# Optimization experiments

Hardware: AMD Instinct MI355X
Metric: run time of the kernel (lower is better)

The kernel has to match this reference:

```python
import jax, jax.numpy as jnp
import numpy as np

NUM_GRAPHS = 512
NODES_PER_GRAPH = 128
HIDDEN = 64
K = 24


def _param(key, shape, scale=0.05):
    return jax.random.normal(key, shape, dtype=jnp.float32) * scale


def setup_inputs() -> dict:
    key = jax.random.key(0)
    ks = jax.random.split(key, 24)
    N = NUM_GRAPHS * NODES_PER_GRAPH
    inp = {
        "x_pf": jax.random.normal(ks[0], (N, 4), dtype=jnp.float32),
        "batch_pf": jnp.repeat(jnp.arange(NUM_GRAPHS, dtype=jnp.int64), NODES_PER_GRAPH),
        # pf_encode: Linear(4,64), ELU, Linear(64,64), ELU
        "we1": _param(ks[1], (4, HIDDEN)), "be1": _param(ks[2], (HIDDEN,)),
        "we2": _param(ks[3], (HIDDEN, HIDDEN)), "be2": _param(ks[4], (HIDDEN,)),
        # three DynamicEdgeConv edge MLPs: Linear(128,64)+ELU
        "wc1": _param(ks[5], (2 * HIDDEN, HIDDEN)), "bc1": _param(ks[6], (HIDDEN,)),
        "wc2": _param(ks[7], (2 * HIDDEN, HIDDEN)), "bc2": _param(ks[8], (HIDDEN,)),
        "wc3": _param(ks[9], (2 * HIDDEN, HIDDEN)), "bc3": _param(ks[10], (HIDDEN,)),
        # output MLP 64->64->32->32->8->1
        "wo1": _param(ks[11], (HIDDEN, 64)), "bo1": _param(ks[12], (64,)),
        "wo2": _param(ks[13], (64, 32)), "bo2": _param(ks[14], (32,)),
        "wo3": _param(ks[15], (32, 32)), "bo3": _param(ks[16], (32,)),
        "wo4": _param(ks[17], (32, 8)), "bo4": _param(ks[18], (8,)),
        "wo5": _param(ks[19], (8, 1)), "bo5": _param(ks[20], (1,)),
    }
    return inp


def dynamic_edge_conv(x, wc, bc):
    """x: [G,P,D]. kNN (incl. self) in feature space per graph, edge feature
    [x_i, x_j - x_i] -> Linear+ELU -> max over neighbors. Matches PyG
    DynamicEdgeConv(nn, k, aggr='max')."""
    sq = jnp.sum(x * x, axis=-1)                                   # [G,P]
    d = sq[:, :, None] + sq[:, None, :] - 2.0 * jnp.einsum('gpd,gqd->gpq', x, x)
    _, idx = jax.lax.top_k(-d, K)                                   # [G,P,K] nearest (self included, dist 0)
    xj = jax.vmap(lambda xg, ig: xg[ig])(x, idx)                    # [G,P,K,D]
    xi = x[:, :, None, :]
    e = jnp.concatenate([jnp.broadcast_to(xi, xj.shape), xj - xi], axis=-1)  # [G,P,K,2D]
    h = jax.nn.elu(e @ wc + bc)                                     # [G,P,K,D]
    return jnp.max(h, axis=2)                                       # [G,P,D]


def reference(x_pf, batch_pf, we1, be1, we2, be2, wc1, bc1, wc2, bc2, wc3, bc3,
              wo1, bo1, wo2, bo2, wo3, bo3, wo4, bo4, wo5, bo5):
    elu = jax.nn.elu
    h = elu(elu(x_pf @ we1 + be1) @ we2 + be2)                      # [N,64]
    h = h.reshape(NUM_GRAPHS, NODES_PER_GRAPH, HIDDEN)              # equal-size graphs
    h = dynamic_edge_conv(h, wc1, bc1)
    h = dynamic_edge_conv(h, wc2, bc2)
    h = dynamic_edge_conv(h, wc3, bc3)
    pooled = jnp.sum(h, axis=1)                                     # global_add_pool -> [G,64]
    o = elu(pooled @ wo1 + bo1)
    o = elu(o @ wo2 + bo2)
    o = elu(o @ wo3 + bo3)
    o = elu(o @ wo4 + bo4)
    out = o @ wo5 + bo5                                             # [G,1]
    return (out, batch_pf)
```

## Files before the change

### kernel.cpp

```cpp
#include <hip/hip_runtime.h>
#include <math.h>

#define NG 512
#define NP 128
#define HID 64
#define KNN 24
#define NTOT (NG*NP)

typedef __attribute__((ext_vector_type(8)))  short  short8;
typedef __attribute__((ext_vector_type(16))) float  floatx16;

__device__ __forceinline__ float elu_f(float v) { return v > 0.0f ? v : expm1f(v); }

__device__ __forceinline__ void split_bf16(float x, unsigned short& hb, unsigned short& lb) {
    unsigned u = __float_as_uint(x);
    unsigned h = (u + 0x7FFFu + ((u >> 16) & 1u)) >> 16;
    hb = (unsigned short)h;
    float hf = __uint_as_float(h << 16);
    float lo = x - hf;
    unsigned v = __float_as_uint(lo);
    lb = (unsigned short)((v + 0x7FFFu + ((v >> 16) & 1u)) >> 16);
}

__device__ __forceinline__ unsigned short* hchunk(unsigned short* base, int row, int ch) {
    return base + (((row << 4) + (ch ^ (row & 15))) << 3);
}
__device__ __forceinline__ const unsigned short* hchunk(const unsigned short* base, int row, int ch) {
    return base + (((row << 4) + (ch ^ (row & 15))) << 3);
}

__device__ __forceinline__ void sort8_asc(unsigned* y) {
    #pragma unroll
    for (int k = 2; k <= 8; k <<= 1)
        #pragma unroll
        for (int j = k >> 1; j > 0; j >>= 1)
            #pragma unroll
            for (int i = 0; i < 8; ++i) {
                const int l = i ^ j;
                if (l > i) {
                    const bool up = ((i & k) == 0);
                    const unsigned a = y[i], b = y[l];
                    const unsigned mn = a < b ? a : b;
                    const unsigned mx = a < b ? b : a;
                    y[i] = up ? mn : mx;
                    y[l] = up ? mx : mn;
                }
            }
}

__device__ __forceinline__ void merge_top24(unsigned* x) {
    #pragma unroll
    for (int d = 16; d > 0; d >>= 1)
        #pragma unroll
        for (int i = 0; i < 32; ++i)
            if (!(i & d) && i < 24) {
                const int l = i | d;
                const unsigned a = x[i], b = x[l];
                x[i] = a < b ? a : b;
                x[l] = a < b ? b : a;
            }
}

__global__ __launch_bounds__(256) void pack_w(
    const float* __restrict__ wc1, const float* __restrict__ wc2, const float* __restrict__ wc3,
    const float* __restrict__ we2,
    unsigned short* __restrict__ wp)
{
    const int n = blockIdx.x*256 + threadIdx.x;
    if (n < 24576) {
        const int layer = n >> 13;
        const int r = n & 8191;
        const int e = r & 7, j = (r >> 3) & 127, ch = r >> 10;
        const int k = (ch >> 1)*16 + (ch & 1)*8 + e;
        const float* wc = (layer == 0) ? wc1 : ((layer == 1) ? wc2 : wc3);
        float w;
        if (j < 64) w = wc[k*64 + j] - wc[(k+64)*64 + j];
        else        w = wc[(k+64)*64 + (j-64)];
        unsigned short hb, lb;
        split_bf16(w, hb, lb);
        unsigned short* base = wp + layer*16384;
        base[r] = hb;
        base[8192 + r] = lb;
    } else if (n < 24576 + 4096) {
        const int m = n - 24576;
        const int e = m & 7, col = (m >> 3) & 63, ch = m >> 9;
        const int k = (ch >> 1)*16 + (ch & 1)*8 + e;
        unsigned short hb, lb;
        split_bf16(we2[k*64 + col], hb, lb);
        unsigned short* base = wp + 49152;
        base[m] = hb;
        base[4096 + m] = lb;
    }
}

template <bool FIRST>
__global__ __launch_bounds__(256, 3) void conv_fused(
    float* __restrict__ h,
    const unsigned short* __restrict__ wp,
    const float* __restrict__ bc,
    float* __restrict__ ag_all,
    const float* __restrict__ x,
    const float* __restrict__ we1, const float* __restrict__ be1,
    const unsigned short* __restrict__ we2p,
    const float* __restrict__ be2,
    float* __restrict__ out_batch)
{
    __shared__ __align__(16) char arena[51712];
    unsigned*        keys = (unsigned*)arena;
    unsigned short*  hilo = (unsigned short*)(arena + 18432);
    float*           sqs  = (float*)(arena + 51200);

    const int g = blockIdx.x;
    const int t = threadIdx.x;
    const int lane = t & 63, w = t >> 6;
    const int lj = lane & 31, half = lane >> 5;
    const int i2 = t & 127, jh = t >> 7;
    float* __restrict__ hg = h + (size_t)g * (NP*HID);
    float* __restrict__ ag = ag_all + (size_t)g * (NP*HID);

    if (FIRST) {
        float* w1s = (float*)arena;
        float* b1v = (float*)(arena + 1024);
        float* b2v = (float*)(arena + 1280);
        w1s[t] = we1[t];
        if (t < 64) { b1v[t] = be1[t]; b2v[t] = be2[t]; }
        if (t < 128) out_batch[(size_t)g*128 + t] = (float)g;
        __syncthreads();

        const int n = t & 127, fh = t >> 7, f0 = fh*32;
        const float4 xv = ((const float4*)x)[g*128 + n];
        float acc1[32];
        #pragma unroll
        for (int q = 0; q < 8; ++q) {
            const float4 b4 = *(const float4*)(b1v + f0 + q*4);
            acc1[q*4+0] = b4.x; acc1[q*4+1] = b4.y; acc1[q*4+2] = b4.z; acc1[q*4+3] = b4.w;
        }
        #pragma unroll
        for (int k = 0; k < 4; ++k) {
            const float xk = (k == 0) ? xv.x : (k == 1) ? xv.y : (k == 2) ? xv.z : xv.w;
            #pragma unroll
            for (int q = 0; q < 8; ++q) {
                const float4 w4 = *(const float4*)(w1s + k*64 + f0 + q*4);
                acc1[q*4+0] = fmaf(xk, w4.x, acc1[q*4+0]);
                acc1[q*4+1] = fmaf(xk, w4.y, acc1[q*4+1]);
                acc1[q*4+2] = fmaf(xk, w4.z, acc1[q*4+2]);
                acc1[q*4+3] = fmaf(xk, w4.w, acc1[q*4+3]);
            }
        }
        unsigned hiw[16], low[16];
        #pragma unroll
        for (int q = 0; q < 16; ++q) {
            const float v0 = elu_f(acc1[2*q]), v1 = elu_f(acc1[2*q+1]);
            unsigned short h0, l0, h1, l1;
            split_bf16(v0, h0, l0); split_bf16(v1, h1, l1);
            hiw[q] = (unsigned)h0 | ((unsigned)h1 << 16);
            low[q] = (unsigned)l0 | ((unsigned)l1 << 16);
        }
        #pragma unroll
        for (int q = 0; q < 4; ++q) {
            *(uint4*)hchunk(hilo, n, fh*4 + q)     = make_uint4(hiw[q*4], hiw[q*4+1], hiw[q*4+2], hiw[q*4+3]);
            *(uint4*)hchunk(hilo, n, 8 + fh*4 + q) = make_uint4(low[q*4], low[q*4+1], low[q*4+2], low[q*4+3]);
        }
        __syncthreads();

        #pragma unroll 1
        for (int jt = 0; jt < 2; ++jt) {
            short8 afr[8], bfr[8];
            #pragma unroll
            for (int sel = 0; sel < 2; ++sel)
                #pragma unroll
                for (int c = 0; c < 4; ++c) {
                    afr[sel*4+c] = *(const short8*)hchunk(hilo, w*32 + lj, sel*8 + c*2 + half);
                    bfr[sel*4+c] = *(const short8*)((const short*)we2p + sel*4096 + (((c*2 + half)*64) + jt*32 + lj)*8);
                }
            floatx16 acc = {0.f,0.f,0.f,0.f,0.f,0.f,0.f,0.f,0.f,0.f,0.f,0.f,0.f,0.f,0.f,0.f};
            #pragma unroll
            for (int c = 0; c < 4; ++c) acc = __builtin_amdgcn_mfma_f32_32x32x16_bf16(afr[c],   bfr[c],   acc, 0, 0, 0);
            #pragma unroll
            for (int c = 0; c < 4; ++c) acc = __builtin_amdgcn_mfma_f32_32x32x16_bf16(afr[c],   bfr[4+c], acc, 0, 0, 0);
            #pragma unroll
            for (int c = 0; c < 4; ++c) acc = __builtin_amdgcn_mfma_f32_32x32x16_bf16(afr[4+c], bfr[c],   acc, 0, 0, 0);
            const int col = jt*32 + lj;
            const float bias = b2v[col];
            #pragma unroll
            for (int reg = 0; reg < 16; ++reg) {
                const int row = (reg & 3) + 8*(reg >> 2) + 4*half + w*32;
                hg[(size_t)row*64 + col] = elu_f(acc[reg] + bias);
            }
        }
        __syncthreads();
    }

    {
        const int r = t >> 1, cb = (t & 1) * 4;
        const float4* src = (const float4*)(hg + r*64 + cb*8);
        unsigned hh[16], llo[16];
        float s = 0.0f;
        #pragma unroll
        for (int q = 0; q < 8; ++q) {
            const float4 v = src[q];
            s = fmaf(v.x, v.x, s); s = fmaf(v.y, v.y, s);
            s = fmaf(v.z, v.z, s); s = fmaf(v.w, v.w, s);
            unsigned short hx, lx, hy, ly, hz, lz, hw2, lw2;
            split_bf16(v.x, hx, lx); split_bf16(v.y, hy, ly);
            split_bf16(v.z, hz, lz); split_bf16(v.w, hw2, lw2);
            hh[q*2]   = (unsigned)hx | ((unsigned)hy << 16);
            hh[q*2+1] = (unsigned)hz | ((unsigned)hw2 << 16);
            llo[q*2]   = (unsigned)lx | ((unsigned)ly << 16);
            llo[q*2+1] = (unsigned)lz | ((unsigned)lw2 << 16);
        }
        #pragma unroll
        for (int q = 0; q < 4; ++q) {
            *(uint4*)hchunk(hilo, r, cb + q)     = make_uint4(hh[q*4], hh[q*4+1], hh[q*4+2], hh[q*4+3]);
            *(uint4*)hchunk(hilo, r, 8 + cb + q) = make_uint4(llo[q*4], llo[q*4+1], llo[q*4+2], llo[q*4+3]);
        }
        s += __shfl_xor(s, 1);
        if ((t & 1) == 0) sqs[r] = s;
    }
    __syncthreads();

    unsigned xk[32];
    #pragma unroll
    for (int s = 0; s < 24; ++s) xk[s] = 0xFFFFFFFFu;

    #pragma unroll 1
    for (int jt = 0; jt < 4; ++jt) {
        short8 afr[8], bfr[8];
        #pragma unroll
        for (int sel = 0; sel < 2; ++sel)
            #pragma unroll
            for (int c = 0; c < 4; ++c) {
                afr[sel*4+c] = *(const short8*)hchunk(hilo, w*32 + lj,  sel*8 + c*2 + half);
                bfr[sel*4+c] = *(const short8*)hchunk(hilo, jt*32 + lj, sel*8 + c*2 + half);
            }
        floatx16 acc = {0.f,0.f,0.f,0.f,0.f,0.f,0.f,0.f,0.f,0.f,0.f,0.f,0.f,0.f,0.f,0.f};
        #pragma unroll
        for (int c = 0; c < 4; ++c) acc = __builtin_amdgcn_mfma_f32_32x32x16_bf16(afr[c],   bfr[c],   acc, 0, 0, 0);
        #pragma unroll
        for (int c = 0; c < 4; ++c) acc = __builtin_amdgcn_mfma_f32_32x32x16_bf16(afr[c],   bfr[4+c], acc, 0, 0, 0);
        #pragma unroll
        for (int c = 0; c < 4; ++c) acc = __builtin_amdgcn_mfma_f32_32x32x16_bf16(afr[4+c], bfr[c],   acc, 0, 0, 0);

        const unsigned jg = (unsigned)(jt*32 + lj);
        const float sqj = sqs[jg];
        #pragma unroll
        for (int reg = 0; reg < 16; ++reg) {
            const int i = (reg & 3) + 8*(reg >> 2) + 4*half + w*32;
            float d = fmaf(-2.0f, acc[reg], sqs[i] + sqj);
            d = fmaxf(d, 0.0f);
            keys[i*36 + lj] = (__float_as_uint(d) & 0xFFFFFF80u) | jg;
        }
        __syncthreads();

        const unsigned* kr = keys + i2*36 + jh*16;
        #pragma unroll
        for (int b = 0; b < 2; ++b) {
            const uint4 k0 = *(const uint4*)(kr + b*8);
            const uint4 k1 = *(const uint4*)(kr + b*8 + 4);
            unsigned y[8] = {k0.x, k0.y, k0.z, k0.w, k1.x, k1.y, k1.z, k1.w};
            sort8_asc(y);
            #pragma unroll
            for (int e = 0; e < 8; ++e) xk[24+e] = y[7-e];
            merge_top24(xk);
        }
        __syncthreads();
    }

    if (jh) {
        #pragma unroll
        for (int s = 0; s < 24; ++s) keys[i2*36 + s] = xk[s];
    }
    __syncthreads();
    if (!jh) {
        #pragma unroll
        for (int b = 0; b < 3; ++b) {
            #pragma unroll
            for (int e = 0; e < 8; ++e) xk[24+e] = keys[i2*36 + b*8 + (7-e)];
            merge_top24(xk);
        }
        #pragma unroll
        for (int c = 0; c < 6; ++c)
            keys[i2*36 + 30 + c] = (xk[c*4] & 127u) | ((xk[c*4+1] & 127u) << 8)
                                 | ((xk[c*4+2] & 127u) << 16) | ((xk[c*4+3] & 127u) << 24);
    }
    __syncthreads();

    float* bs = (float*)(arena + 18432);
    {
        short8 afr[8];
        #pragma unroll
        for (int sel = 0; sel < 2; ++sel)
            #pragma unroll
            for (int c = 0; c < 4; ++c)
                afr[sel*4+c] = *(const short8*)hchunk(hilo, w*32 + lj, sel*8 + c*2 + half);
        __syncthreads();

        #pragma unroll 1
        for (int jt = 0; jt < 4; ++jt) {
            short8 bfr[8];
            #pragma unroll
            for (int part = 0; part < 2; ++part)
                #pragma unroll
                for (int c = 0; c < 4; ++c)
                    bfr[part*4+c] = *(const short8*)((const short*)wp + part*8192 + (((c*2 + half)*128) + jt*32 + lj)*8);
            floatx16 acc = {0.f,0.f,0.f,0.f,0.f,0.f,0.f,0.f,0.f,0.f,0.f,0.f,0.f,0.f,0.f,0.f};
            #pragma unroll
            for (int c = 0; c < 4; ++c) acc = __builtin_amdgcn_mfma_f32_32x32x16_bf16(afr[c],   bfr[c],   acc, 0, 0, 0);
            #pragma unroll
            for (int c = 0; c < 4; ++c) acc = __builtin_amdgcn_mfma_f32_32x32x16_bf16(afr[c],   bfr[4+c], acc, 0, 0, 0);
            #pragma unroll
            for (int c = 0; c < 4; ++c) acc = __builtin_amdgcn_mfma_f32_32x32x16_bf16(afr[4+c], bfr[c],   acc, 0, 0, 0);

            if (jt < 2) {
                const int col = jt*32 + lj;
                const float bias = bc[col];
                #pragma unroll
                for (int reg = 0; reg < 16; ++reg) {
                    const int row = (reg & 3) + 8*(reg >> 2) + 4*half + w*32;
                    ag[(size_t)row*64 + col] = acc[reg] + bias;
                }
            } else {
                const int colb = (jt - 2)*32 + lj;
                #pragma unroll
                for (int reg = 0; reg < 16; ++reg) {
                    const int row = (reg & 3) + 8*(reg >> 2) + 4*half + w*32;
                    bs[row*64 + colb] = acc[reg];
                }
            }
        }
    }
    __syncthreads();

    {
        const int q = lane >> 4, fq = lane & 15;
        float4 av[8];
        #pragma unroll
        for (int rg = 0; rg < 8; ++rg)
            av[rg] = *(const float4*)(ag + (size_t)(w*32 + rg*4 + q)*64 + fq*4);
        #pragma unroll 1
        for (int rg = 0; rg < 8; ++rg) {
            const int row = w*32 + rg*4 + q;
            float4 m = make_float4(-1e30f, -1e30f, -1e30f, -1e30f);
            #pragma unroll
            for (int c = 0; c < 6; ++c) {
                const unsigned pk = keys[row*36 + 30 + c];
                #pragma unroll
                for (int e = 0; e < 4; ++e) {
                    const int j = (pk >> (8*e)) & 127;
                    const float4 v = *(const float4*)(bs + j*64 + fq*4);
                    m.x = fmaxf(m.x, v.x); m.y = fmaxf(m.y, v.y);
                    m.z = fmaxf(m.z, v.z); m.w = fmaxf(m.w, v.w);
                }
            }
            float4 o;
            o.x = elu_f(av[rg].x + m.x); o.y = elu_f(av[rg].y + m.y);
            o.z = elu_f(av[rg].z + m.z); o.w = elu_f(av[rg].w + m.w);
            *(float4*)(hg + (size_t)row*64 + fq*4) = o;
        }
    }
}

__global__ __launch_bounds__(256) void head_kernel(
    const float* __restrict__ h,
    const float* __restrict__ wo1, const float* __restrict__ bo1,
    const float* __restrict__ wo2, const float* __restrict__ bo2,
    const float* __restrict__ wo3, const float* __restrict__ bo3,
    const float* __restrict__ wo4, const float* __restrict__ bo4,
    const float* __restrict__ wo5, const float* __restrict__ bo5,
    float* __restrict__ outp)
{
    __shared__ float pool4[4][64];
    __shared__ float pooled[64];
    __shared__ float o1[64];
    __shared__ float o2[32];
    __shared__ float o3[32];
    __shared__ float o4[8];
    const int g = blockIdx.x, t = threadIdx.x;
    const int f = t & 63, q = t >> 6;
    const float* __restrict__ hg = h + (size_t)g * (NP*HID);

    float s = 0.0f;
    #pragma unroll 8
    for (int n = q; n < NP; n += 4) s += hg[n*64 + f];
    pool4[q][f] = s;
    __syncthreads();

    if (t < 64) {
        pooled[t] = pool4[0][t] + pool4[1][t] + pool4[2][t] + pool4[3][t];
        {
            float acc = bo1[t];
            #pragma unroll
            for (int k = 0; k < 64; ++k) acc = fmaf(pooled[k], wo1[k*64 + t], acc);
            o1[t] = elu_f(acc);
        }
        if (t < 32) {
            float acc = bo2[t];
            #pragma unroll
            for (int k = 0; k < 64; ++k) acc = fmaf(o1[k], wo2[k*32 + t], acc);
            o2[t] = elu_f(acc);
        }
        if (t < 32) {
            float acc = bo3[t];
            #pragma unroll
            for (int k = 0; k < 32; ++k) acc = fmaf(o2[k], wo3[k*32 + t], acc);
            o3[t] = elu_f(acc);
        }
        if (t < 8) {
            float acc = bo4[t];
            #pragma unroll
            for (int k = 0; k < 32; ++k) acc = fmaf(o3[k], wo4[k*8 + t], acc);
            o4[t] = elu_f(acc);
        }
        if (t == 0) {
            float acc = bo5[0];
            #pragma unroll
            for (int k = 0; k < 8; ++k) acc = fmaf(o4[k], wo5[k], acc);
            outp[g] = acc;
        }
    }
}

extern "C" void kernel_launch(void* const* d_in, const int* in_sizes, int n_in,
                              void* d_out, int out_size, void* d_ws, size_t ws_size,
                              hipStream_t stream) {
    const float* x_pf = (const float*)d_in[0];
    const float* we1 = (const float*)d_in[2];
    const float* be1 = (const float*)d_in[3];
    const float* we2 = (const float*)d_in[4];
    const float* be2 = (const float*)d_in[5];
    const float* wc1 = (const float*)d_in[6];
    const float* bc1 = (const float*)d_in[7];
    const float* wc2 = (const float*)d_in[8];
    const float* bc2 = (const float*)d_in[9];
    const float* wc3 = (const float*)d_in[10];
    const float* bc3 = (const float*)d_in[11];
    const float* wo1 = (const float*)d_in[12];
    const float* bo1 = (const float*)d_in[13];
    const float* wo2 = (const float*)d_in[14];
    const float* bo2 = (const float*)d_in[15];
    const float* wo3 = (const float*)d_in[16];
    const float* bo3 = (const float*)d_in[17];
    const float* wo4 = (const float*)d_in[18];
    const float* bo4 = (const float*)d_in[19];
    const float* wo5 = (const float*)d_in[20];
    const float* bo5 = (const float*)d_in[21];

    float* out = (float*)d_out;
    char* ws = (char*)d_ws;
    float* h0 = (float*)(ws);
    float* abuf = (float*)(ws + (size_t)16*1024*1024);
    unsigned short* wpack = (unsigned short*)(ws + (size_t)32*1024*1024);

    pack_w<<<112, 256, 0, stream>>>(wc1, wc2, wc3, we2, wpack);

    conv_fused<true><<<NG, 256, 0, stream>>>(h0, wpack, bc1, abuf,
        x_pf, we1, be1, wpack + 49152, be2, out + NG);
    conv_fused<false><<<NG, 256, 0, stream>>>(h0, wpack + 16384, bc2, abuf,
        nullptr, nullptr, nullptr, nullptr, nullptr, nullptr);
    conv_fused<false><<<NG, 256, 0, stream>>>(h0, wpack + 32768, bc3, abuf,
        nullptr, nullptr, nullptr, nullptr, nullptr, nullptr);

    head_kernel<<<NG, 256, 0, stream>>>(h0, wo1, bo1, wo2, bo2, wo3, bo3, wo4, bo4, wo5, bo5, out);
}
```

Before: 207.1 us.

## Fuse encoder, three edge-conv layers and pooling into one 512-thread kernel

Merges the encoder and all three DynamicEdgeConv layers into a single kernel per graph, launched with 512 threads. Node features stay in LDS as split bf16 hi/lo between layers instead of round-tripping through global memory. Global add pooling now happens inside the fused kernel, so the head only reads 64 pooled values per graph. This removes two kernel launches and the per-layer global reads and writes of features. The costs are a larger LDS footprint, bf16-stored neighbor projections that may shift precision, and more intra-block synchronisation for the four-way top-k merge.

```diff
diff --git a/kernel.cpp b/kernel.cpp
--- a/kernel.cpp
+++ b/kernel.cpp
@@ -21,6 +21,12 @@
     unsigned v = __float_as_uint(lo);
     lb = (unsigned short)((v + 0x7FFFu + ((v >> 16) & 1u)) >> 16);
 }
+__device__ __forceinline__ unsigned short bf_rne(float x) {
+    unsigned u = __float_as_uint(x);
+    return (unsigned short)((u + 0x7FFFu + ((u >> 16) & 1u)) >> 16);
+}
+__device__ __forceinline__ float bf_lo(unsigned u) { return __uint_as_float(u << 16); }
+__device__ __forceinline__ float bf_hi(unsigned u) { return __uint_as_float(u & 0xFFFF0000u); }
 
 __device__ __forceinline__ unsigned short* hchunk(unsigned short* base, int row, int ch) {
     return base + (((row << 4) + (ch ^ (row & 15))) << 3);
@@ -93,275 +99,308 @@
     }
 }
 
-template <bool FIRST>
-__global__ __launch_bounds__(256, 3) void conv_fused(
-    float* __restrict__ h,
+__global__ __launch_bounds__(512, 4) void conv_all(
+    const float* __restrict__ x,
     const unsigned short* __restrict__ wp,
-    const float* __restrict__ bc,
-    float* __restrict__ ag_all,
-    const float* __restrict__ x,
+    const float* __restrict__ bc1, const float* __restrict__ bc2, const float* __restrict__ bc3,
     const float* __restrict__ we1, const float* __restrict__ be1,
-    const unsigned short* __restrict__ we2p,
-    const float* __restrict__ be2,
-    float* __restrict__ out_batch)
+    const unsigned short* __restrict__ we2p, const float* __restrict__ be2,
+    float* __restrict__ ag_all, float* __restrict__ pooled_out, float* __restrict__ out_batch)
 {
-    __shared__ __align__(16) char arena[51712];
-    unsigned*        keys = (unsigned*)arena;
-    unsigned short*  hilo = (unsigned short*)(arena + 18432);
-    float*           sqs  = (float*)(arena + 51200);
+    __shared__ __align__(16) char arena[54784];
+    unsigned*        keys  = (unsigned*)arena;
+    unsigned*        nnidx = (unsigned*)(arena + 18432);
+    unsigned short*  hilo  = (unsigned short*)(arena + 21504);
+    float*           sqs   = (float*)(arena + 54272);
 
     const int g = blockIdx.x;
     const int t = threadIdx.x;
-    const int lane = t & 63, w = t >> 6;
+    const int w = t >> 6, lane = t & 63;
     const int lj = lane & 31, half = lane >> 5;
-    const int i2 = t & 127, jh = t >> 7;
-    float* __restrict__ hg = h + (size_t)g * (NP*HID);
+    const int rt = w & 3, wg = w >> 2;
+    const int i2 = t & 127, s4 = t >> 7;
     float* __restrict__ ag = ag_all + (size_t)g * (NP*HID);
 
-    if (FIRST) {
+    {
         float* w1s = (float*)arena;
         float* b1v = (float*)(arena + 1024);
         float* b2v = (float*)(arena + 1280);
-        w1s[t] = we1[t];
-        if (t < 64) { b1v[t] = be1[t]; b2v[t] = be2[t]; }
+        if (t < 256) w1s[t] = we1[t];
+        else if (t < 320) b1v[t-256] = be1[t-256];
+        else if (t < 384) b2v[t-320] = be2[t-320];
         if (t < 128) out_batch[(size_t)g*128 + t] = (float)g;
         __syncthreads();
 
-        const int n = t & 127, fh = t >> 7, f0 = fh*32;
+        const int n = t & 127, fh = t >> 7, f0 = fh*16;
         const float4 xv = ((const float4*)x)[g*128 + n];
-        float acc1[32];
-        #pragma unroll
-        for (int q = 0; q < 8; ++q) {
+        float acc1[16];
+        #pragma unroll
+        for (int q = 0; q < 4; ++q) {
             const float4 b4 = *(const float4*)(b1v + f0 + q*4);
             acc1[q*4+0] = b4.x; acc1[q*4+1] = b4.y; acc1[q*4+2] = b4.z; acc1[q*4+3] = b4.w;
         }
         #pragma unroll
         for (int k = 0; k < 4; ++k) {
-            const float xk = (k == 0) ? xv.x : (k == 1) ? xv.y : (k == 2) ? xv.z : xv.w;
-            #pragma unroll
-            for (int q = 0; q < 8; ++q) {
+            const float xk_ = (k == 0) ? xv.x : (k == 1) ? xv.y : (k == 2) ? xv.z : xv.w;
+            #pragma unroll
+            for (int q = 0; q < 4; ++q) {
                 const float4 w4 = *(const float4*)(w1s + k*64 + f0 + q*4);
-                acc1[q*4+0] = fmaf(xk, w4.x, acc1[q*4+0]);
-                acc1[q*4+1] = fmaf(xk, w4.y, acc1[q*4+1]);
-                acc1[q*4+2] = fmaf(xk, w4.z, acc1[q*4+2]);
-                acc1[q*4+3] = fmaf(xk, w4.w, acc1[q*4+3]);
-            }
-        }
-        unsigned hiw[16], low[16];
-        #pragma unroll
-        for (int q = 0; q < 16; ++q) {
-            const float v0 = elu_f(acc1[2*q]), v1 = elu_f(acc1[2*q+1]);
+                acc1[q*4+0] = fmaf(xk_, w4.x, acc1[q*4+0]);
+                acc1[q*4+1] = fmaf(xk_, w4.y, acc1[q*4+1]);
+                acc1[q*4+2] = fmaf(xk_, w4.z, acc1[q*4+2]);
+                acc1[q*4+3] = fmaf(xk_, w4.w, acc1[q*4+3]);
+            }
+        }
+        unsigned hu[8], lu[8];
+        #pragma unroll
+        for (int e = 0; e < 8; ++e) {
+            const float v0 = elu_f(acc1[2*e]), v1 = elu_f(acc1[2*e+1]);
             unsigned short h0, l0, h1, l1;
             split_bf16(v0, h0, l0); split_bf16(v1, h1, l1);
-            hiw[q] = (unsigned)h0 | ((unsigned)h1 << 16);
-            low[q] = (unsigned)l0 | ((unsigned)l1 << 16);
-        }
-        #pragma unroll
-        for (int q = 0; q < 4; ++q) {
-            *(uint4*)hchunk(hilo, n, fh*4 + q)     = make_uint4(hiw[q*4], hiw[q*4+1], hiw[q*4+2], hiw[q*4+3]);
-            *(uint4*)hchunk(hilo, n, 8 + fh*4 + q) = make_uint4(low[q*4], low[q*4+1], low[q*4+2], low[q*4+3]);
-        }
-        __syncthreads();
-
-        #pragma unroll 1
-        for (int jt = 0; jt < 2; ++jt) {
-            short8 afr[8], bfr[8];
-            #pragma unroll
-            for (int sel = 0; sel < 2; ++sel)
-                #pragma unroll
-                for (int c = 0; c < 4; ++c) {
-                    afr[sel*4+c] = *(const short8*)hchunk(hilo, w*32 + lj, sel*8 + c*2 + half);
-                    bfr[sel*4+c] = *(const short8*)((const short*)we2p + sel*4096 + (((c*2 + half)*64) + jt*32 + lj)*8);
-                }
-            floatx16 acc = {0.f,0.f,0.f,0.f,0.f,0.f,0.f,0.f,0.f,0.f,0.f,0.f,0.f,0.f,0.f,0.f};
-            #pragma unroll
-            for (int c = 0; c < 4; ++c) acc = __builtin_amdgcn_mfma_f32_32x32x16_bf16(afr[c],   bfr[c],   acc, 0, 0, 0);
-            #pragma unroll
-            for (int c = 0; c < 4; ++c) acc = __builtin_amdgcn_mfma_f32_32x32x16_bf16(afr[c],   bfr[4+c], acc, 0, 0, 0);
-            #pragma unroll
-            for (int c = 0; c < 4; ++c) acc = __builtin_amdgcn_mfma_f32_32x32x16_bf16(afr[4+c], bfr[c],   acc, 0, 0, 0);
-            const int col = jt*32 + lj;
-            const float bias = b2v[col];
-            #pragma unroll
-            for (int reg = 0; reg < 16; ++reg) {
-                const int row = (reg & 3) + 8*(reg >> 2) + 4*half + w*32;
-                hg[(size_t)row*64 + col] = elu_f(acc[reg] + bias);
-            }
-        }
-        __syncthreads();
-    }
-
-    {
-        const int r = t >> 1, cb = (t & 1) * 4;
-        const float4* src = (const float4*)(hg + r*64 + cb*8);
-        unsigned hh[16], llo[16];
+            hu[e] = (unsigned)h0 | ((unsigned)h1 << 16);
+            lu[e] = (unsigned)l0 | ((unsigned)l1 << 16);
+        }
+        *(uint4*)hchunk(hilo, n, fh*2)       = make_uint4(hu[0], hu[1], hu[2], hu[3]);
+        *(uint4*)hchunk(hilo, n, fh*2 + 1)   = make_uint4(hu[4], hu[5], hu[6], hu[7]);
+        *(uint4*)hchunk(hilo, n, 8 + fh*2)   = make_uint4(lu[0], lu[1], lu[2], lu[3]);
+        *(uint4*)hchunk(hilo, n, 8 + fh*2+1) = make_uint4(lu[4], lu[5], lu[6], lu[7]);
+        __syncthreads();
+
+        const int jt2 = wg;
+        floatx16 acc = {0.f,0.f,0.f,0.f,0.f,0.f,0.f,0.f,0.f,0.f,0.f,0.f,0.f,0.f,0.f,0.f};
+        #pragma unroll
+        for (int p = 0; p < 3; ++p) {
+            const int aSel = (p == 2) ? 8 : 0;
+            const int part = (p == 1) ? 1 : 0;
+            short8 af[4], bf4[4];
+            #pragma unroll
+            for (int c = 0; c < 4; ++c) {
+                af[c]  = *(const short8*)hchunk(hilo, rt*32 + lj, aSel + c*2 + half);
+                bf4[c] = *(const short8*)((const short*)we2p + part*4096 + (((c*2 + half)*64) + jt2*32 + lj)*8);
+            }
+            #pragma unroll
+            for (int c = 0; c < 4; ++c) acc = __builtin_amdgcn_mfma_f32_32x32x16_bf16(af[c], bf4[c], acc, 0, 0, 0);
+        }
+        const int col = jt2*32 + lj;
+        const float bias = b2v[col];
+        __syncthreads();
+        #pragma unroll
+        for (int reg = 0; reg < 16; ++reg) {
+            const int row = (reg & 3) + 8*(reg >> 2) + 4*half + rt*32;
+            const float v = elu_f(acc[reg] + bias);
+            unsigned short hb, lb;
+            split_bf16(v, hb, lb);
+            *(hchunk(hilo, row, col >> 3) + (col & 7))       = hb;
+            *(hchunk(hilo, row, 8 + (col >> 3)) + (col & 7)) = lb;
+        }
+        __syncthreads();
+
+        const int r = t >> 2, cq = t & 3, c0 = cq*2;
+        const uint4 h0 = *(const uint4*)hchunk(hilo, r, c0);
+        const uint4 h1 = *(const uint4*)hchunk(hilo, r, c0+1);
+        const uint4 l0 = *(const uint4*)hchunk(hilo, r, 8+c0);
+        const uint4 l1 = *(const uint4*)hchunk(hilo, r, 8+c0+1);
         float s = 0.0f;
-        #pragma unroll
-        for (int q = 0; q < 8; ++q) {
-            const float4 v = src[q];
-            s = fmaf(v.x, v.x, s); s = fmaf(v.y, v.y, s);
-            s = fmaf(v.z, v.z, s); s = fmaf(v.w, v.w, s);
-            unsigned short hx, lx, hy, ly, hz, lz, hw2, lw2;
-            split_bf16(v.x, hx, lx); split_bf16(v.y, hy, ly);
-            split_bf16(v.z, hz, lz); split_bf16(v.w, hw2, lw2);
-            hh[q*2]   = (unsigned)hx | ((unsigned)hy << 16);
-            hh[q*2+1] = (unsigned)hz | ((unsigned)hw2 << 16);
-            llo[q*2]   = (unsigned)lx | ((unsigned)ly << 16);
-            llo[q*2+1] = (unsigned)lz | ((unsigned)lw2 << 16);
-        }
-        #pragma unroll
-        for (int q = 0; q < 4; ++q) {
-            *(uint4*)hchunk(hilo, r, cb + q)     = make_uint4(hh[q*4], hh[q*4+1], hh[q*4+2], hh[q*4+3]);
-            *(uint4*)hchunk(hilo, r, 8 + cb + q) = make_uint4(llo[q*4], llo[q*4+1], llo[q*4+2], llo[q*4+3]);
+        const unsigned hh[8] = {h0.x,h0.y,h0.z,h0.w,h1.x,h1.y,h1.z,h1.w};
+        const unsigned ll[8] = {l0.x,l0.y,l0.z,l0.w,l1.x,l1.y,l1.z,l1.w};
+        #pragma unroll
+        for (int e = 0; e < 8; ++e) {
+            const float va = bf_lo(hh[e]) + bf_lo(ll[e]);
+            const float vb = bf_hi(hh[e]) + bf_hi(ll[e]);
+            s = fmaf(va, va, s); s = fmaf(vb, vb, s);
         }
         s += __shfl_xor(s, 1);
-        if ((t & 1) == 0) sqs[r] = s;
-    }
-    __syncthreads();
-
-    unsigned xk[32];
-    #pragma unroll
-    for (int s = 0; s < 24; ++s) xk[s] = 0xFFFFFFFFu;
+        s += __shfl_xor(s, 2);
+        if (cq == 0) sqs[r] = s;
+        __syncthreads();
+    }
 
     #pragma unroll 1
-    for (int jt = 0; jt < 4; ++jt) {
-        short8 afr[8], bfr[8];
-        #pragma unroll
-        for (int sel = 0; sel < 2; ++sel)
-            #pragma unroll
-            for (int c = 0; c < 4; ++c) {
-                afr[sel*4+c] = *(const short8*)hchunk(hilo, w*32 + lj,  sel*8 + c*2 + half);
-                bfr[sel*4+c] = *(const short8*)hchunk(hilo, jt*32 + lj, sel*8 + c*2 + half);
-            }
-        floatx16 acc = {0.f,0.f,0.f,0.f,0.f,0.f,0.f,0.f,0.f,0.f,0.f,0.f,0.f,0.f,0.f,0.f};
-        #pragma unroll
-        for (int c = 0; c < 4; ++c) acc = __builtin_amdgcn_mfma_f32_32x32x16_bf16(afr[c],   bfr[c],   acc, 0, 0, 0);
-        #pragma unroll
-        for (int c = 0; c < 4; ++c) acc = __builtin_amdgcn_mfma_f32_32x32x16_bf16(afr[c],   bfr[4+c], acc, 0, 0, 0);
-        #pragma unroll
-        for (int c = 0; c < 4; ++c) acc = __builtin_amdgcn_mfma_f32_32x32x16_bf16(afr[4+c], bfr[c],   acc, 0, 0, 0);
-
-        const unsigned jg = (unsigned)(jt*32 + lj);
-        const float sqj = sqs[jg];
-        #pragma unroll
-        for (int reg = 0; reg < 16; ++reg) {
-            const int i = (reg & 3) + 8*(reg >> 2) + 4*half + w*32;
-            float d = fmaf(-2.0f, acc[reg], sqs[i] + sqj);
-            d = fmaxf(d, 0.0f);
-            keys[i*36 + lj] = (__float_as_uint(d) & 0xFFFFFF80u) | jg;
-        }
-        __syncthreads();
-
-        const unsigned* kr = keys + i2*36 + jh*16;
-        #pragma unroll
-        for (int b = 0; b < 2; ++b) {
-            const uint4 k0 = *(const uint4*)(kr + b*8);
-            const uint4 k1 = *(const uint4*)(kr + b*8 + 4);
-            unsigned y[8] = {k0.x, k0.y, k0.z, k0.w, k1.x, k1.y, k1.z, k1.w};
-            sort8_asc(y);
-            #pragma unroll
-            for (int e = 0; e < 8; ++e) xk[24+e] = y[7-e];
-            merge_top24(xk);
-        }
-        __syncthreads();
-    }
-
-    if (jh) {
-        #pragma unroll
-        for (int s = 0; s < 24; ++s) keys[i2*36 + s] = xk[s];
-    }
-    __syncthreads();
-    if (!jh) {
-        #pragma unroll
-        for (int b = 0; b < 3; ++b) {
-            #pragma unroll
-            for (int e = 0; e < 8; ++e) xk[24+e] = keys[i2*36 + b*8 + (7-e)];
-            merge_top24(xk);
-        }
-        #pragma unroll
-        for (int c = 0; c < 6; ++c)
-            keys[i2*36 + 30 + c] = (xk[c*4] & 127u) | ((xk[c*4+1] & 127u) << 8)
-                                 | ((xk[c*4+2] & 127u) << 16) | ((xk[c*4+3] & 127u) << 24);
-    }
-    __syncthreads();
-
-    float* bs = (float*)(arena + 18432);
-    {
-        short8 afr[8];
-        #pragma unroll
-        for (int sel = 0; sel < 2; ++sel)
-            #pragma unroll
-            for (int c = 0; c < 4; ++c)
-                afr[sel*4+c] = *(const short8*)hchunk(hilo, w*32 + lj, sel*8 + c*2 + half);
-        __syncthreads();
+    for (int L = 0; L < 3; ++L) {
+        const unsigned short* wpl = wp + L*16384;
+        const float* bcl = (L == 0) ? bc1 : (L == 1) ? bc2 : bc3;
+
+        unsigned xk[32];
+        #pragma unroll
+        for (int s = 0; s < 24; ++s) xk[s] = 0xFFFFFFFFu;
 
         #pragma unroll 1
         for (int jt = 0; jt < 4; ++jt) {
-            short8 bfr[8];
-            #pragma unroll
-            for (int part = 0; part < 2; ++part)
+            if (wg == (jt & 1)) {
+                floatx16 acc = {0.f,0.f,0.f,0.f,0.f,0.f,0.f,0.f,0.f,0.f,0.f,0.f,0.f,0.f,0.f,0.f};
+                #pragma unroll
+                for (int p = 0; p < 3; ++p) {
+                    const int aSel = (p == 2) ? 8 : 0;
+                    const int bSel = (p == 1) ? 8 : 0;
+                    short8 af[4], bf4[4];
+                    #pragma unroll
+                    for (int c = 0; c < 4; ++c) {
+                        af[c]  = *(const short8*)hchunk(hilo, rt*32 + lj, aSel + c*2 + half);
+                        bf4[c] = *(const short8*)hchunk(hilo, jt*32 + lj, bSel + c*2 + half);
+                    }
+                    #pragma unroll
+                    for (int c = 0; c < 4; ++c) acc = __builtin_amdgcn_mfma_f32_32x32x16_bf16(af[c], bf4[c], acc, 0, 0, 0);
+                }
+                const unsigned jg = (unsigned)(jt*32 + lj);
+                const float sqj = sqs[jg];
+                #pragma unroll
+                for (int reg = 0; reg < 16; ++reg) {
+                    const int i = (reg & 3) + 8*(reg >> 2) + 4*half + rt*32;
+                    float d = fmaf(-2.0f, acc[reg], sqs[i] + sqj);
+                    d = fmaxf(d, 0.0f);
+                    keys[i*36 + lj] = (__float_as_uint(d) & 0xFFFFFF80u) | jg;
+                }
+            }
+            __syncthreads();
+            {
+                const unsigned* kr = keys + i2*36 + s4*8;
+                const uint4 k0 = *(const uint4*)kr;
+                const uint4 k1 = *(const uint4*)(kr + 4);
+                unsigned y[8] = {k0.x, k0.y, k0.z, k0.w, k1.x, k1.y, k1.z, k1.w};
+                sort8_asc(y);
+                #pragma unroll
+                for (int e = 0; e < 8; ++e) xk[24+e] = y[7-e];
+                merge_top24(xk);
+            }
+            __syncthreads();
+        }
+
+        #pragma unroll 1
+        for (int src = 1; src < 4; ++src) {
+            if (s4 == src) {
+                #pragma unroll
+                for (int e = 0; e < 24; ++e) keys[i2*36 + 12 + e] = xk[e];
+            }
+            __syncthreads();
+            if (s4 == 0) {
+                #pragma unroll 1
+                for (int b = 0; b < 3; ++b) {
+                    #pragma unroll
+                    for (int e = 0; e < 8; ++e) xk[24+e] = keys[i2*36 + 12 + b*8 + (7-e)];
+                    merge_top24(xk);
+                }
+            }
+            __syncthreads();
+        }
+        if (s4 == 0) {
+            #pragma unroll
+            for (int c = 0; c < 6; ++c)
+                nnidx[i2*6 + c] = (xk[c*4] & 127u) | ((xk[c*4+1] & 127u) << 8)
+                                | ((xk[c*4+2] & 127u) << 16) | ((xk[c*4+3] & 127u) << 24);
+        }
+        __syncthreads();
+
+        unsigned short* bs = (unsigned short*)arena;
+        {
+            short8 afr[8];
+            #pragma unroll
+            for (int sel = 0; sel < 2; ++sel)
                 #pragma unroll
                 for (int c = 0; c < 4; ++c)
-                    bfr[part*4+c] = *(const short8*)((const short*)wp + part*8192 + (((c*2 + half)*128) + jt*32 + lj)*8);
-            floatx16 acc = {0.f,0.f,0.f,0.f,0.f,0.f,0.f,0.f,0.f,0.f,0.f,0.f,0.f,0.f,0.f,0.f};
-            #pragma unroll
-            for (int c = 0; c < 4; ++c) acc = __builtin_amdgcn_mfma_f32_32x32x16_bf16(afr[c],   bfr[c],   acc, 0, 0, 0);
-            #pragma unroll
-            for (int c = 0; c < 4; ++c) acc = __builtin_amdgcn_mfma_f32_32x32x16_bf16(afr[c],   bfr[4+c], acc, 0, 0, 0);
-            #pragma unroll
-            for (int c = 0; c < 4; ++c) acc = __builtin_amdgcn_mfma_f32_32x32x16_bf16(afr[4+c], bfr[c],   acc, 0, 0, 0);
-
-            if (jt < 2) {
-                const int col = jt*32 + lj;
-                const float bias = bc[col];
-                #pragma unroll
-                for (int reg = 0; reg < 16; ++reg) {
-                    const int row = (reg & 3) + 8*(reg >> 2) + 4*half + w*32;
-                    ag[(size_t)row*64 + col] = acc[reg] + bias;
-                }
+                    afr[sel*4+c] = *(const short8*)hchunk(hilo, rt*32 + lj, sel*8 + c*2 + half);
+
+            #pragma unroll 1
+            for (int q2 = 0; q2 < 2; ++q2) {
+                const int jt = wg*2 + q2;
+                short8 bfr[8];
+                #pragma unroll
+                for (int part = 0; part < 2; ++part)
+                    #pragma unroll
+                    for (int c = 0; c < 4; ++c)
+                        bfr[part*4+c] = *(const short8*)((const short*)wpl + part*8192 + (((c*2 + half)*128) + jt*32 + lj)*8);
+                floatx16 acc = {0.f,0.f,0.f,0.f,0.f,0.f,0.f,0.f,0.f,0.f,0.f,0.f,0.f,0.f,0.f,0.f};
+                #pragma unroll
+                for (int c = 0; c < 4; ++c) acc = __builtin_amdgcn_mfma_f32_32x32x16_bf16(afr[c],   bfr[c],   acc, 0, 0, 0);
+                #pragma unroll
+                for (int c = 0; c < 4; ++c) acc = __builtin_amdgcn_mfma_f32_32x32x16_bf16(afr[c],   bfr[4+c], acc, 0, 0, 0);
+                #pragma unroll
+                for (int c = 0; c < 4; ++c) acc = __builtin_amdgcn_mfma_f32_32x32x16_bf16(afr[4+c], bfr[c],   acc, 0, 0, 0);
+
+                if (wg == 0) {
+                    const int col = jt*32 + lj;
+                    const float bias = bcl[col];
+                    #pragma unroll
+                    for (int reg = 0; reg < 16; ++reg) {
+                        const int row = (reg & 3) + 8*(reg >> 2) + 4*half + rt*32;
+                        ag[(size_t)row*64 + col] = acc[reg] + bias;
+                    }
+                } else {
+                    const int colb = q2*32 + lj;
+                    #pragma unroll
+                    for (int reg = 0; reg < 16; ++reg) {
+                        const int row = (reg & 3) + 8*(reg >> 2) + 4*half + rt*32;
+                        bs[row*68 + colb] = bf_rne(acc[reg]);
+                    }
+                }
+            }
+        }
+        __syncthreads();
+
+        {
+            const int q = lane >> 4, fq = lane & 15;
+            float4 psum = make_float4(0.f, 0.f, 0.f, 0.f);
+            #pragma unroll 1
+            for (int rg = 0; rg < 4; ++rg) {
+                const int row = w*16 + rg*4 + q;
+                float4 m = make_float4(-3e38f, -3e38f, -3e38f, -3e38f);
+                #pragma unroll
+                for (int c = 0; c < 6; ++c) {
+                    const unsigned pk = nnidx[row*6 + c];
+                    #pragma unroll
+                    for (int e = 0; e < 4; ++e) {
+                        const int j = (pk >> (8*e)) & 127;
+                        const uint2 bb = *(const uint2*)(bs + j*68 + fq*4);
+                        m.x = fmaxf(m.x, bf_lo(bb.x)); m.y = fmaxf(m.y, bf_hi(bb.x));
+                        m.z = fmaxf(m.z, bf_lo(bb.y)); m.w = fmaxf(m.w, bf_hi(bb.y));
+                    }
+                }
+                const float4 av = *(const float4*)(ag + (size_t)row*64 + fq*4);
+                float4 o;
+                o.x = elu_f(av.x + m.x); o.y = elu_f(av.y + m.y);
+                o.z = elu_f(av.z + m.z); o.w = elu_f(av.w + m.w);
+
+                if (L < 2) {
+                    unsigned short hx,lx,hy,ly,hz,lz,hw2,lw2;
+                    split_bf16(o.x,hx,lx); split_bf16(o.y,hy,ly);
+                    split_bf16(o.z,hz,lz); split_bf16(o.w,hw2,lw2);
+                    *(uint2*)(hchunk(hilo, row, fq >> 1) + (fq & 1)*4) =
+                        make_uint2((unsigned)hx | ((unsigned)hy << 16), (unsigned)hz | ((unsigned)hw2 << 16));
+                    *(uint2*)(hchunk(hilo, row, 8 + (fq >> 1)) + (fq & 1)*4) =
+                        make_uint2((unsigned)lx | ((unsigned)ly << 16), (unsigned)lz | ((unsigned)lw2 << 16));
+                    float sp = o.x*o.x + o.y*o.y + o.z*o.z + o.w*o.w;
+                    sp += __shfl_xor(sp, 1);
+                    sp += __shfl_xor(sp, 2);
+                    sp += __shfl_xor(sp, 4);
+                    sp += __shfl_xor(sp, 8);
+                    if (fq == 0) sqs[row] = sp;
+                } else {
+                    psum.x += o.x; psum.y += o.y; psum.z += o.z; psum.w += o.w;
+                }
+            }
+            if (L < 2) {
+                __syncthreads();
             } else {
-                const int colb = (jt - 2)*32 + lj;
-                #pragma unroll
-                for (int reg = 0; reg < 16; ++reg) {
-                    const int row = (reg & 3) + 8*(reg >> 2) + 4*half + w*32;
-                    bs[row*64 + colb] = acc[reg];
-                }
-            }
-        }
-    }
-    __syncthreads();
-
-    {
-        const int q = lane >> 4, fq = lane & 15;
-        float4 av[8];
-        #pragma unroll
-        for (int rg = 0; rg < 8; ++rg)
-            av[rg] = *(const float4*)(ag + (size_t)(w*32 + rg*4 + q)*64 + fq*4);
-        #pragma unroll 1
-        for (int rg = 0; rg < 8; ++rg) {
-            const int row = w*32 + rg*4 + q;
-            float4 m = make_float4(-1e30f, -1e30f, -1e30f, -1e30f);
-            #pragma unroll
-            for (int c = 0; c < 6; ++c) {
-                const unsigned pk = keys[row*36 + 30 + c];
-                #pragma unroll
-                for (int e = 0; e < 4; ++e) {
-                    const int j = (pk >> (8*e)) & 127;
-                    const float4 v = *(const float4*)(bs + j*64 + fq*4);
-                    m.x = fmaxf(m.x, v.x); m.y = fmaxf(m.y, v.y);
-                    m.z = fmaxf(m.z, v.z); m.w = fmaxf(m.w, v.w);
-                }
-            }
-            float4 o;
-            o.x = elu_f(av[rg].x + m.x); o.y = elu_f(av[rg].y + m.y);
-            o.z = elu_f(av[rg].z + m.z); o.w = elu_f(av[rg].w + m.w);
-            *(float4*)(hg + (size_t)row*64 + fq*4) = o;
-        }
-    }
-}
-
-__global__ __launch_bounds__(256) void head_kernel(
-    const float* __restrict__ h,
+                __syncthreads();
+                float* pool8 = (float*)(arena + 18432);
+                psum.x += __shfl_xor(psum.x, 16); psum.y += __shfl_xor(psum.y, 16);
+                psum.z += __shfl_xor(psum.z, 16); psum.w += __shfl_xor(psum.w, 16);
+                psum.x += __shfl_xor(psum.x, 32); psum.y += __shfl_xor(psum.y, 32);
+                psum.z += __shfl_xor(psum.z, 32); psum.w += __shfl_xor(psum.w, 32);
+                if (q == 0) *(float4*)(pool8 + w*64 + fq*4) = psum;
+                __syncthreads();
+                if (t < 64) {
+                    float s = 0.0f;
+                    #pragma unroll
+                    for (int k = 0; k < 8; ++k) s += pool8[k*64 + t];
+                    pooled_out[(size_t)g*64 + t] = s;
+                }
+            }
+        }
+    }
+}
+
+__global__ __launch_bounds__(64) void head_kernel(
+    const float* __restrict__ pooled_in,
     const float* __restrict__ wo1, const float* __restrict__ bo1,
     const float* __restrict__ wo2, const float* __restrict__ bo2,
     const float* __restrict__ wo3, const float* __restrict__ bo3,
@@ -369,54 +408,43 @@
     const float* __restrict__ wo5, const float* __restrict__ bo5,
     float* __restrict__ outp)
 {
-    __shared__ float pool4[4][64];
     __shared__ float pooled[64];
     __shared__ float o1[64];
     __shared__ float o2[32];
     __shared__ float o3[32];
     __shared__ float o4[8];
     const int g = blockIdx.x, t = threadIdx.x;
-    const int f = t & 63, q = t >> 6;
-    const float* __restrict__ hg = h + (size_t)g * (NP*HID);
-
-    float s = 0.0f;
-    #pragma unroll 8
-    for (int n = q; n < NP; n += 4) s += hg[n*64 + f];
-    pool4[q][f] = s;
-    __syncthreads();
-
-    if (t < 64) {
-        pooled[t] = pool4[0][t] + pool4[1][t] + pool4[2][t] + pool4[3][t];
-        {
-            float acc = bo1[t];
-            #pragma unroll
-            for (int k = 0; k < 64; ++k) acc = fmaf(pooled[k], wo1[k*64 + t], acc);
-            o1[t] = elu_f(acc);
-        }
-        if (t < 32) {
-            float acc = bo2[t];
-            #pragma unroll
-            for (int k = 0; k < 64; ++k) acc = fmaf(o1[k], wo2[k*32 + t], acc);
-            o2[t] = elu_f(acc);
-        }
-        if (t < 32) {
-            float acc = bo3[t];
-            #pragma unroll
-            for (int k = 0; k < 32; ++k) acc = fmaf(o2[k], wo3[k*32 + t], acc);
-            o3[t] = elu_f(acc);
-        }
-        if (t < 8) {
-            float acc = bo4[t];
-            #pragma unroll
-            for (int k = 0; k < 32; ++k) acc = fmaf(o3[k], wo4[k*8 + t], acc);
-            o4[t] = elu_f(acc);
-        }
-        if (t == 0) {
-            float acc = bo5[0];
-            #pragma unroll
-            for (int k = 0; k < 8; ++k) acc = fmaf(o4[k], wo5[k], acc);
-            outp[g] = acc;
-        }
+
+    pooled[t] = pooled_in[(size_t)g*64 + t];
+    {
+        float acc = bo1[t];
+        #pragma unroll
+        for (int k = 0; k < 64; ++k) acc = fmaf(pooled[k], wo1[k*64 + t], acc);
+        o1[t] = elu_f(acc);
+    }
+    if (t < 32) {
+        float acc = bo2[t];
+        #pragma unroll
+        for (int k = 0; k < 64; ++k) acc = fmaf(o1[k], wo2[k*32 + t], acc);
+        o2[t] = elu_f(acc);
+    }
+    if (t < 32) {
+        float acc = bo3[t];
+        #pragma unroll
+        for (int k = 0; k < 32; ++k) acc = fmaf(o2[k], wo3[k*32 + t], acc);
+        o3[t] = elu_f(acc);
+    }
+    if (t < 8) {
+        float acc = bo4[t];
+        #pragma unroll
+        for (int k = 0; k < 32; ++k) acc = fmaf(o3[k], wo4[k*8 + t], acc);
+        o4[t] = elu_f(acc);
+    }
+    if (t == 0) {
+        float acc = bo5[0];
+        #pragma unroll
+        for (int k = 0; k < 8; ++k) acc = fmaf(o4[k], wo5[k], acc);
+        outp[g] = acc;
     }
 }
 
@@ -447,18 +475,14 @@
 
     float* out = (float*)d_out;
     char* ws = (char*)d_ws;
-    float* h0 = (float*)(ws);
-    float* abuf = (float*)(ws + (size_t)16*1024*1024);
-    unsigned short* wpack = (unsigned short*)(ws + (size_t)32*1024*1024);
+    float* abuf   = (float*)(ws);
+    float* pooled = (float*)(ws + (size_t)16*1024*1024);
+    unsigned short* wpack = (unsigned short*)(ws + (size_t)17*1024*1024);
 
     pack_w<<<112, 256, 0, stream>>>(wc1, wc2, wc3, we2, wpack);
 
-    conv_fused<true><<<NG, 256, 0, stream>>>(h0, wpack, bc1, abuf,
-        x_pf, we1, be1, wpack + 49152, be2, out + NG);
-    conv_fused<false><<<NG, 256, 0, stream>>>(h0, wpack + 16384, bc2, abuf,
-        nullptr, nullptr, nullptr, nullptr, nullptr, nullptr);
-    conv_fused<false><<<NG, 256, 0, stream>>>(h0, wpack + 32768, bc3, abuf,
-        nullptr, nullptr, nullptr, nullptr, nullptr, nullptr);
-
-    head_kernel<<<NG, 256, 0, stream>>>(h0, wo1, bo1, wo2, bo2, wo3, bo3, wo4, bo4, wo5, bo5, out);
-}
+    conv_all<<<NG, 512, 0, stream>>>(x_pf, wpack, bc1, bc2, bc3,
+        we1, be1, wpack + 49152, be2, abuf, pooled, out + NG);
+
+    head_kernel<<<NG, 64, 0, stream>>>(pooled, wo1, bo1, wo2, bo2, wo3, bo3, wo4, bo4, wo5, bo5, out);
+}
```

Result: faster. 189.1 us (-8.7%).
